# Kernel tuning notes

Hardware: AMD Instinct MI355X
Metric: run time of the kernel (lower is better)

## Reference

```python
import jax, jax.numpy as jnp
import numpy as np
from jax import lax

EPS = 1e-5

def _conv(x, w, pad):
    # x: NCHW, w: OIHW, stride 1
    return lax.conv_general_dilated(x, w, (1, 1), [(pad, pad), (pad, pad)],
                                    dimension_numbers=('NCHW', 'OIHW', 'NCHW'))

def _binconv(x, w):
    # IR-Net/ReActNet HardBinaryConv: sign-binarized weights scaled by per-filter
    # mean |w| (alpha), sign-binarized activations; clip-based STE for backward.
    alpha = jnp.mean(jnp.abs(w), axis=(1, 2, 3), keepdims=True)  # [O,1,1,1]
    wc = jnp.clip(w, -1.0, 1.0)
    bw = lax.stop_gradient(alpha * jnp.sign(w) - wc) + wc
    xc = jnp.clip(x, -1.0, 1.0)
    ba = lax.stop_gradient(jnp.sign(x) - xc) + xc
    return _conv(ba, bw, 1)

def _bn(x, g, b, m, v):
    # inference-mode BatchNorm2d with running stats
    inv = g / jnp.sqrt(v + EPS)
    return x * inv[None, :, None, None] + (b - m * inv)[None, :, None, None]

def _pool(x):
    return lax.reduce_window(x, -jnp.inf, lax.max, (1, 1, 2, 2), (1, 1, 2, 2), 'VALID')

def _htanh(x):
    return jnp.clip(x, -1.0, 1.0)

def setup_inputs() -> dict:
    key = jax.random.key(0)
    ks = jax.random.split(key, 40)
    B = 256
    d = {'x': jax.random.normal(ks[0], (B, 3, 32, 32), jnp.float32)}
    shapes = [(128, 3, 3, 3), (128, 128, 3, 3), (256, 128, 3, 3),
              (256, 256, 3, 3), (512, 256, 3, 3), (512, 512, 3, 3)]
    chans = [128, 128, 256, 256, 512, 512]
    ki = 1
    for i, (ws, c) in enumerate(zip(shapes, chans)):
        fan_in = ws[1] * 9
        d[f'w{i}'] = jax.random.normal(ks[ki], ws, jnp.float32) / np.sqrt(fan_in); ki += 1
        d[f'g{i}'] = jnp.ones((c,), jnp.float32)
        d[f'b{i}'] = jnp.zeros((c,), jnp.float32)
        d[f'm{i}'] = jax.random.normal(ks[ki], (c,), jnp.float32) * 0.1; ki += 1
        d[f'v{i}'] = jax.random.uniform(ks[ki], (c,), jnp.float32, 0.5, 1.5); ki += 1
    d['fcw'] = jax.random.normal(ks[ki], (10, 512 * 4 * 4), jnp.float32) * 0.01
    d['fcb'] = jnp.zeros((10,), jnp.float32)
    return d

def reference(x, w0, g0, b0, m0, v0, w1, g1, b1, m1, v1, w2, g2, b2, m2, v2,
              w3, g3, b3, m3, v3, w4, g4, b4, m4, v4, w5, g5, b5, m5, v5,
              fcw, fcb):
    h = _bn(_conv(x, w0, 1), g0, b0, m0, v0)            # [B,128,32,32]
    h = _htanh(_bn(_pool(_binconv(h, w1)), g1, b1, m1, v1))   # [B,128,16,16]
    h = _htanh(_bn(_binconv(h, w2), g2, b2, m2, v2))          # [B,256,16,16]
    h = _htanh(_bn(_pool(_binconv(h, w3)), g3, b3, m3, v3))   # [B,256,8,8]
    h = _htanh(_bn(_binconv(h, w4), g4, b4, m4, v4))          # [B,512,8,8]
    h = _htanh(_bn(_pool(_binconv(h, w5)), g5, b5, m5, v5))   # [B,512,4,4]
    h = h.reshape(h.shape[0], -1)                             # [B,8192]
    return h @ fcw.T + fcb                                    # [B,10]
```

## Files before the change

kernel.cpp:

```cpp
#include <hip/hip_runtime.h>
#include <cstdint>

#define EPS 1e-5
typedef unsigned long long u64;
typedef unsigned int u32;

struct BnArgs { const float *g[6], *b[6], *m[6], *v[6]; };
struct PackArgs { const float* w[5]; u64* wbt[5]; };

__global__ void bn_prep_all(BnArgs p, double* __restrict__ scale_all,
                            double* __restrict__ shift_all) {
    int i = blockIdx.x * 256 + threadIdx.x;
    if (i >= 1792) return;
    int l, base;
    if (i < 128)       { l = 0; base = 0; }
    else if (i < 256)  { l = 1; base = 128; }
    else if (i < 512)  { l = 2; base = 256; }
    else if (i < 768)  { l = 3; base = 512; }
    else if (i < 1280) { l = 4; base = 768; }
    else               { l = 5; base = 1280; }
    const int c = i - base;
    double inv = (double)p.g[l][c] / sqrt((double)p.v[l][c] + EPS);
    scale_all[i] = inv;
    shift_all[i] = (double)p.b[l][c] - (double)p.m[l][c] * inv;
}

__global__ void zero_out(float* __restrict__ out, int n) {
    int i = blockIdx.x * blockDim.x + threadIdx.x;
    if (i < n) out[i] = 0.f;
}

__global__ void zero_u64(u64* __restrict__ p, size_t n) {
    size_t i = (size_t)blockIdx.x * 256 + threadIdx.x;
    const size_t step = (size_t)gridDim.x * 256;
    for (; i < n; i += step) p[i] = 0ull;
}

__global__ void pack_all(PackArgs pk, const double* __restrict__ scale_all,
                         double* __restrict__ A_all, u32* __restrict__ ct_all) {
    const int ob = blockIdx.x;
    const int t = threadIdx.x;
    int l, base, Cin, bnoff, OTOT, ctoff;
    if (ob < 128)       { l = 0; base = 0;    Cin = 128; bnoff = 128;  OTOT = 128; ctoff = 0; }
    else if (ob < 384)  { l = 1; base = 128;  Cin = 128; bnoff = 256;  OTOT = 256; ctoff = 2048; }
    else if (ob < 640)  { l = 2; base = 384;  Cin = 256; bnoff = 512;  OTOT = 256; ctoff = 6144; }
    else if (ob < 1152) { l = 3; base = 640;  Cin = 256; bnoff = 768;  OTOT = 512; ctoff = 10240; }
    else                { l = 4; base = 1152; Cin = 512; bnoff = 1280; OTOT = 512; ctoff = 18432; }
    const int o = ob - base;
    const float* wo = pk.w[l] + (size_t)o * Cin * 9;

    double s = 0.0;
    for (int k = t; k < Cin * 9; k += 256) s += fabs((double)wo[k]);
    __shared__ double red[256];
    __shared__ u32 stp[9];
    red[t] = s;
    if (t < 9) stp[t] = 0;
    __syncthreads();
    for (int r = 128; r > 0; r >>= 1) {
        if (t < r) red[t] += red[t + r];
        __syncthreads();
    }
    if (t == 0) {
        double alpha = red[0] / (double)(Cin * 9);
        A_all[ob] = alpha * scale_all[bnoff + o];
    }

    const int W64 = Cin / 64;
    u64* wbt = pk.wbt[l];
    for (int e = t; e < 9 * W64; e += 256) {
        int tap = e / W64, word = e % W64;
        u64 bits = 0;
        for (int j = 0; j < 64; ++j) {
            int c = word * 64 + j;
            if (wo[c * 9 + tap] < 0.f) bits |= (1ull << j);
        }
        wbt[((size_t)tap * OTOT + o) * W64 + word] = bits;
        atomicAdd(&stp[tap], (u32)__popcll(bits));
    }
    __syncthreads();

    if (t < 16) {
        const int pat = t;
        int nv = 0;
        u32 cor = 0;
#pragma unroll
        for (int tap = 0; tap < 9; ++tap) {
            const int dy = tap / 3, dx = tap % 3;
            const bool inv = ((pat & 1) && dy == 0) || ((pat & 2) && dy == 2) ||
                             ((pat & 4) && dx == 0) || ((pat & 8) && dx == 2);
            if (inv) cor += stp[tap]; else nv++;
        }
        ct_all[ctoff + pat * OTOT + o] = (u32)(nv * 64 * W64) + 2u * cor;
    }
}

__global__ __launch_bounds__(256) void conv0_pack(
        const float* __restrict__ x, const float* __restrict__ w0,
        const double* __restrict__ scale, const double* __restrict__ shift,
        u64* __restrict__ bits0) {
    __shared__ double wlds[128 * 27];
    __shared__ double sc[128], sh[128];
    const int tid = threadIdx.x;
    for (int e = tid; e < 128 * 27; e += 256) wlds[e] = (double)w0[e];
    for (int e = tid; e < 128; e += 256) { sc[e] = scale[e]; sh[e] = shift[e]; }
    __syncthreads();

    const int n = blockIdx.y;
    const int p = blockIdx.x * 256 + tid;
    const int y = p >> 5, xx = p & 31;
    const float* xn = x + (size_t)n * 3 * 32 * 32;

    double win[27];
#pragma unroll
    for (int c = 0; c < 3; ++c)
#pragma unroll
        for (int dy = 0; dy < 3; ++dy)
#pragma unroll
            for (int dx = 0; dx < 3; ++dx) {
                const int yy = y + dy - 1, xs = xx + dx - 1;
                const bool ok = (yy >= 0 && yy < 32 && xs >= 0 && xs < 32);
                win[(c * 3 + dy) * 3 + dx] = ok ? (double)xn[(c * 32 + yy) * 32 + xs] : 0.0;
            }

    u64* op = bits0 + (((size_t)n * 34 + (y + 1)) * 34 + (xx + 1)) * 2;
#pragma unroll
    for (int og = 0; og < 2; ++og) {
        u64 word = 0;
#pragma unroll 2
        for (int j = 0; j < 64; ++j) {
            const int o = og * 64 + j;
            const double* wo = &wlds[o * 27];
            double acc = 0.0;
#pragma unroll
            for (int k = 0; k < 27; ++k) acc = fma(wo[k], win[k], acc);
            const double val = acc * sc[o] + sh[o];
            word |= (u64)(val < 0.0) << j;
        }
        op[og] = word;
    }
}

template<int H, int W, int W64, int OTOT, bool POOL, bool LAST, int MINW>
__global__ __launch_bounds__(256, MINW) void bconv6(
        const u64* __restrict__ in_bits, const u64* __restrict__ wbt,
        const double* __restrict__ A, const double* __restrict__ B,
        const u32* __restrict__ ct_all, int ctoff,
        u32* __restrict__ out_bits, float* __restrict__ h5) {
    const int tid = threadIdx.x;
    const int wave = tid >> 6, lane = tid & 63;
    constexpr int OPW = 32;
    constexpr int WPI = (H * W) / 64;
    constexpr int IPB = (WPI >= 4) ? 1 : (4 / WPI);
    const int img = (IPB == 1) ? blockIdx.z : blockIdx.z * IPB + wave;
    const int wii = (IPB == 1) ? (blockIdx.y * 4 + wave) : 0;
    const int y = wii * (64 / W) + lane / W;
    const int x = lane % W;
    const int obase = blockIdx.x * OPW;

    __shared__ u64 wl[9 * OPW * W64];
    __shared__ u32 ctl[16 * 33];
    __shared__ double Ald[OPW], Bld[OPW];
    {
        for (int e = tid; e < 9 * OPW * W64; e += 256) {
            const int tap = e / (OPW * W64), r = e % (OPW * W64);
            wl[e] = wbt[((size_t)tap * OTOT + obase) * W64 + r];
        }
        for (int e = tid; e < 16 * OPW; e += 256) {
            const int pat = e >> 5, oc = e & 31;
            ctl[pat * 33 + oc] = ct_all[ctoff + pat * OTOT + obase + oc];
        }
        for (int e = tid; e < OPW; e += 256) {
            Ald[e] = A[obase + e];
            Bld[e] = B[obase + e];
        }
    }
    __syncthreads();

    constexpr int RC = W + 2;
    const u64* ib = in_bits + (size_t)img * (H + 2) * RC * W64;

    int acc[OPW];
#pragma unroll
    for (int i = 0; i < OPW; ++i) acc[i] = 0;

#pragma unroll 1
    for (int dy = 0; dy < 3; ++dy) {
#pragma unroll 1
        for (int dx = 0; dx < 3; ++dx) {
            const u64* q = ib + ((size_t)(y + dy) * RC + (x + dx)) * W64;
            u64 wn[W64];
#pragma unroll
            for (int k = 0; k < W64; ++k) wn[k] = q[k];
            const u64* wt = &wl[(dy * 3 + dx) * OPW * W64];
#pragma unroll
            for (int oc = 0; oc < OPW; ++oc) {
#pragma unroll
                for (int k = 0; k < W64; ++k)
                    acc[oc] += (int)__popcll(wn[k] ^ wt[oc * W64 + k]);
            }
        }
    }

    const int pat = (y == 0 ? 1 : 0) | (y == H - 1 ? 2 : 0) |
                    (x == 0 ? 4 : 0) | (x == W - 1 ? 8 : 0);
    const int ctbase = pat * 33;
    constexpr int Hp = POOL ? H / 2 : H, Wp = POOL ? W / 2 : W;
    const bool writer = (!POOL) || (((lane & 1) == 0) && ((lane & W) == 0));
    const int py = POOL ? (y >> 1) : y, px = POOL ? (x >> 1) : x;

    u32 cur = 0;
#pragma unroll
    for (int oc = 0; oc < OPW; ++oc) {
        int v = (int)ctl[ctbase + oc] - 2 * acc[oc];
        if (POOL) {
            int v2 = max(v, __shfl_xor(v, 1, 64));
            v = max(v2, __shfl_xor(v2, W, 64));
        }
        const double t = fma(Ald[oc], (double)v, Bld[oc]);
        if (LAST) {
            const double hcl = fmin(1.0, fmax(-1.0, t));
            if (writer)
                h5[(((size_t)img * OTOT + obase + oc) * Hp + py) * Wp + px] = (float)hcl;
        } else {
            cur |= (u32)(t < 0.0) << oc;
        }
    }
    if (!LAST && writer) {
        out_bits[(((size_t)img * (Hp + 2) + (py + 1)) * (Wp + 2) + (px + 1)) * (OTOT / 32)
                 + (obase >> 5)] = cur;
    }
}

__global__ void fc_kernel(const float* __restrict__ h, const float* __restrict__ fcw,
                          const float* __restrict__ fcb, float* __restrict__ out) {
    const int n = blockIdx.x, t = threadIdx.x;
    double acc[10];
#pragma unroll
    for (int j = 0; j < 10; ++j) acc[j] = 0.0;
    const float* hn = h + (size_t)n * 8192;
    for (int k = t; k < 8192; k += 256) {
        double xv = (double)hn[k];
#pragma unroll
        for (int j = 0; j < 10; ++j) acc[j] += xv * (double)fcw[j * 8192 + k];
    }
    __shared__ double red[10][256];
#pragma unroll
    for (int j = 0; j < 10; ++j) red[j][t] = acc[j];
    __syncthreads();
    for (int r = 128; r > 0; r >>= 1) {
        if (t < r) {
#pragma unroll
            for (int j = 0; j < 10; ++j) red[j][t] += red[j][t + r];
        }
        __syncthreads();
    }
    if (t < 10) out[n * 10 + t] = (float)(red[t][0] + (double)fcb[t]);
}

extern "C" void kernel_launch(void* const* d_in, const int* in_sizes, int n_in,
                              void* d_out, int out_size, void* d_ws, size_t ws_size,
                              hipStream_t stream) {
    const float* X = (const float*)d_in[0];
    BnArgs bn;
    PackArgs pk;
    const float* Wt0 = (const float*)d_in[1];
    for (int i = 0; i < 6; ++i) {
        bn.g[i] = (const float*)d_in[2 + 5 * i];
        bn.b[i] = (const float*)d_in[3 + 5 * i];
        bn.m[i] = (const float*)d_in[4 + 5 * i];
        bn.v[i] = (const float*)d_in[5 + 5 * i];
    }
    for (int i = 0; i < 5; ++i) pk.w[i] = (const float*)d_in[1 + 5 * (i + 1)];
    const float* fcw = (const float*)d_in[31];
    const float* fcb = (const float*)d_in[32];
    float* out = (float*)d_out;

    char* ws = (char*)d_ws;
    size_t off = 0;
    auto alloc = [&](size_t bytes) -> void* {
        void* p = ws + off;
        off = (off + bytes + 255) & ~(size_t)255;
        return p;
    };

    double* scale_all = (double*)alloc(1792 * sizeof(double));
    double* shift_all = (double*)alloc(1792 * sizeof(double));
    double* A_all     = (double*)alloc(1664 * sizeof(double));
    u32* ct_all       = (u32*)alloc(26624 * sizeof(u32));
    const size_t WBN[5] = {128ull * 9 * 2, 256ull * 9 * 2, 256ull * 9 * 4,
                           512ull * 9 * 4, 512ull * 9 * 8};
    for (int i = 0; i < 5; ++i) pk.wbt[i] = (u64*)alloc(WBN[i] * sizeof(u64));
    u64* bits4 = (u64*)alloc(256ull * 10 * 10 * 8 * sizeof(u64));
    u64* bits0 = (u64*)alloc(256ull * 34 * 34 * 2 * sizeof(u64));
    u64* bits1 = (u64*)alloc(256ull * 18 * 18 * 2 * sizeof(u64));
    u64* bits2 = (u64*)alloc(256ull * 18 * 18 * 4 * sizeof(u64));
    u64* bits3 = (u64*)alloc(256ull * 10 * 10 * 4 * sizeof(u64));
    const size_t bits_u64 =
        256ull * (10 * 10 * 8 + 34 * 34 * 2 + 18 * 18 * 2 + 18 * 18 * 4 + 10 * 10 * 4);
    float* h5 = (float*)bits0;
    {
        const size_t h5_bytes = 256ull * 8192 * sizeof(float);
        const size_t have = (size_t)((char*)(bits3 + 256ull * 10 * 10 * 4) - (char*)bits0);
        if (h5_bytes > have) alloc(h5_bytes - have);
    }

    if (off > ws_size) {
        zero_out<<<dim3((out_size + 255) / 256), dim3(256), 0, stream>>>(out, out_size);
        return;
    }

    const int BOF[6] = {0, 128, 256, 512, 768, 1280};
    const int AOF[5] = {0, 128, 384, 640, 1152};
    const int CTO[5] = {0, 2048, 6144, 10240, 18432};

    bn_prep_all<<<dim3(7), dim3(256), 0, stream>>>(bn, scale_all, shift_all);
    pack_all<<<dim3(1664), dim3(256), 0, stream>>>(pk, scale_all, A_all, ct_all);
    zero_u64<<<dim3(2048), dim3(256), 0, stream>>>(bits4, bits_u64);

    conv0_pack<<<dim3(4, 256), dim3(256), 0, stream>>>(
        X, Wt0, scale_all + BOF[0], shift_all + BOF[0], bits0);

    bconv6<32, 32, 2, 128, true, false, 4><<<dim3(4, 4, 256), dim3(256), 0, stream>>>(
        bits0, pk.wbt[0], A_all + AOF[0], shift_all + BOF[1], ct_all, CTO[0],
        (u32*)bits1, nullptr);
    bconv6<16, 16, 2, 256, false, false, 4><<<dim3(8, 1, 256), dim3(256), 0, stream>>>(
        bits1, pk.wbt[1], A_all + AOF[1], shift_all + BOF[2], ct_all, CTO[1],
        (u32*)bits2, nullptr);
    bconv6<16, 16, 4, 256, true, false, 4><<<dim3(8, 1, 256), dim3(256), 0, stream>>>(
        bits2, pk.wbt[2], A_all + AOF[2], shift_all + BOF[3], ct_all, CTO[2],
        (u32*)bits3, nullptr);
    bconv6<8, 8, 4, 512, false, false, 4><<<dim3(16, 1, 64), dim3(256), 0, stream>>>(
        bits3, pk.wbt[3], A_all + AOF[3], shift_all + BOF[4], ct_all, CTO[3],
        (u32*)bits4, nullptr);
    bconv6<8, 8, 8, 512, true, true, 4><<<dim3(16, 1, 64), dim3(256), 0, stream>>>(
        bits4, pk.wbt[4], A_all + AOF[4], shift_all + BOF[5], ct_all, CTO[4],
        nullptr, h5);

    fc_kernel<<<dim3(256), dim3(256), 0, stream>>>(h5, fcw, fcb, out);
}
```

Measured before the change: 588.2 us.

## Add quad-per-thread pooled last binary conv and narrow layer-4 channel tiles

The last binary conv layer moves to a new kernel in which each thread computes all four pre-pool pixels of one 2x2 window for 4 output channels. This removes the shuffle-based max pooling and the idle non-writer lanes, and gives 2048 blocks instead of 1024. Layer 4 now uses 16 output channels per block with 16-bit packed output stores, which doubles the block count. The cost is more register use (MINW 2) and more redundant loads of input windows.

After: 609.9 us. 1.04x slower.

```diff
diff --git a/kernel.cpp b/kernel.cpp
--- a/kernel.cpp
+++ b/kernel.cpp
@@ -4,6 +4,7 @@
 #define EPS 1e-5
 typedef unsigned long long u64;
 typedef unsigned int u32;
+typedef unsigned short u16;
 
 struct BnArgs { const float *g[6], *b[6], *m[6], *v[6]; };
 struct PackArgs { const float* w[5]; u64* wbt[5]; };
@@ -140,15 +141,14 @@
     }
 }
 
-template<int H, int W, int W64, int OTOT, bool POOL, bool LAST, int MINW>
+template<int H, int W, int W64, int OTOT, int OPW, bool POOL, int MINW>
 __global__ __launch_bounds__(256, MINW) void bconv6(
         const u64* __restrict__ in_bits, const u64* __restrict__ wbt,
         const double* __restrict__ A, const double* __restrict__ B,
         const u32* __restrict__ ct_all, int ctoff,
-        u32* __restrict__ out_bits, float* __restrict__ h5) {
+        u32* __restrict__ out_bits) {
     const int tid = threadIdx.x;
     const int wave = tid >> 6, lane = tid & 63;
-    constexpr int OPW = 32;
     constexpr int WPI = (H * W) / 64;
     constexpr int IPB = (WPI >= 4) ? 1 : (4 / WPI);
     const int img = (IPB == 1) ? blockIdx.z : blockIdx.z * IPB + wave;
@@ -158,7 +158,7 @@
     const int obase = blockIdx.x * OPW;
 
     __shared__ u64 wl[9 * OPW * W64];
-    __shared__ u32 ctl[16 * 33];
+    __shared__ u32 ctl[16 * (OPW + 1)];
     __shared__ double Ald[OPW], Bld[OPW];
     {
         for (int e = tid; e < 9 * OPW * W64; e += 256) {
@@ -166,8 +166,8 @@
             wl[e] = wbt[((size_t)tap * OTOT + obase) * W64 + r];
         }
         for (int e = tid; e < 16 * OPW; e += 256) {
-            const int pat = e >> 5, oc = e & 31;
-            ctl[pat * 33 + oc] = ct_all[ctoff + pat * OTOT + obase + oc];
+            const int pat = e / OPW, oc = e % OPW;
+            ctl[pat * (OPW + 1) + oc] = ct_all[ctoff + pat * OTOT + obase + oc];
         }
         for (int e = tid; e < OPW; e += 256) {
             Ald[e] = A[obase + e];
@@ -203,7 +203,7 @@
 
     const int pat = (y == 0 ? 1 : 0) | (y == H - 1 ? 2 : 0) |
                     (x == 0 ? 4 : 0) | (x == W - 1 ? 8 : 0);
-    const int ctbase = pat * 33;
+    const int ctbase = pat * (OPW + 1);
     constexpr int Hp = POOL ? H / 2 : H, Wp = POOL ? W / 2 : W;
     const bool writer = (!POOL) || (((lane & 1) == 0) && ((lane & W) == 0));
     const int py = POOL ? (y >> 1) : y, px = POOL ? (x >> 1) : x;
@@ -217,17 +217,106 @@
             v = max(v2, __shfl_xor(v2, W, 64));
         }
         const double t = fma(Ald[oc], (double)v, Bld[oc]);
-        if (LAST) {
-            const double hcl = fmin(1.0, fmax(-1.0, t));
-            if (writer)
-                h5[(((size_t)img * OTOT + obase + oc) * Hp + py) * Wp + px] = (float)hcl;
-        } else {
-            cur |= (u32)(t < 0.0) << oc;
-        }
-    }
-    if (!LAST && writer) {
-        out_bits[(((size_t)img * (Hp + 2) + (py + 1)) * (Wp + 2) + (px + 1)) * (OTOT / 32)
-                 + (obase >> 5)] = cur;
+        cur |= (u32)(t < 0.0) << oc;
+    }
+    if (writer) {
+        const size_t pixbase = ((size_t)img * (Hp + 2) + (py + 1)) * (Wp + 2) + (px + 1);
+        if (OPW == 32)
+            out_bits[pixbase * (OTOT / 32) + (obase >> 5)] = cur;
+        else
+            ((u16*)out_bits)[pixbase * (OTOT / 16) + (obase >> 4)] = (u16)cur;
+    }
+}
+
+template<int MINW>
+__global__ __launch_bounds__(256, MINW) void bconv_quad(
+        const u64* __restrict__ in_bits, const u64* __restrict__ wbt,
+        const double* __restrict__ A, const double* __restrict__ B,
+        const u32* __restrict__ ct_all, int ctoff,
+        float* __restrict__ h5) {
+    constexpr int W64 = 8, OTOT = 512, OPW = 4;
+    const int tid = threadIdx.x;
+    const int wave = tid >> 6, lane = tid & 63;
+    const int img = blockIdx.y * 16 + wave * 4 + (lane >> 4);
+    const int quad = lane & 15;
+    const int py = quad >> 2, px = quad & 3;
+    const int obase = blockIdx.x * OPW;
+
+    __shared__ u64 wl[9 * OPW * W64];
+    __shared__ u32 ctl[16 * (OPW + 1)];
+    __shared__ double Ald[OPW], Bld[OPW];
+    for (int e = tid; e < 9 * OPW * W64; e += 256) {
+        const int tap = e / (OPW * W64), r = e % (OPW * W64);
+        wl[e] = wbt[((size_t)tap * OTOT + obase) * W64 + r];
+    }
+    if (tid < 16 * OPW) {
+        const int pat = tid / OPW, oc = tid % OPW;
+        ctl[pat * (OPW + 1) + oc] = ct_all[ctoff + pat * OTOT + obase + oc];
+    }
+    if (tid < OPW) { Ald[tid] = A[obase + tid]; Bld[tid] = B[obase + tid]; }
+    __syncthreads();
+
+    const u64* ib = in_bits + (size_t)img * 10 * 10 * W64;
+
+    int acc[4][OPW];
+#pragma unroll
+    for (int p = 0; p < 4; ++p)
+#pragma unroll
+        for (int oc = 0; oc < OPW; ++oc) acc[p][oc] = 0;
+
+#pragma unroll 1
+    for (int dy = 0; dy < 3; ++dy) {
+#pragma unroll 1
+        for (int dx = 0; dx < 3; ++dx) {
+            u64 win[2][2][W64];
+#pragma unroll
+            for (int p = 0; p < 2; ++p)
+#pragma unroll
+                for (int q = 0; q < 2; ++q) {
+                    const u64* src = ib + ((size_t)(2 * py + p + dy) * 10 +
+                                           (2 * px + q + dx)) * W64;
+#pragma unroll
+                    for (int k = 0; k < W64; ++k) win[p][q][k] = src[k];
+                }
+            const u64* wt = &wl[(dy * 3 + dx) * OPW * W64];
+#pragma unroll
+            for (int oc = 0; oc < OPW; ++oc) {
+                u64 w[W64];
+#pragma unroll
+                for (int k = 0; k < W64; ++k) w[k] = wt[oc * W64 + k];
+#pragma unroll
+                for (int p = 0; p < 2; ++p)
+#pragma unroll
+                    for (int q = 0; q < 2; ++q) {
+                        int tp = 0;
+#pragma unroll
+                        for (int k = 0; k < W64; ++k)
+                            tp += (int)__popcll(win[p][q][k] ^ w[k]);
+                        acc[p * 2 + q][oc] += tp;
+                    }
+            }
+        }
+    }
+
+    int patp[4];
+#pragma unroll
+    for (int p = 0; p < 2; ++p)
+#pragma unroll
+        for (int q = 0; q < 2; ++q) {
+            const int cy = 2 * py + p, cx = 2 * px + q;
+            patp[p * 2 + q] = (cy == 0 ? 1 : 0) | (cy == 7 ? 2 : 0) |
+                              (cx == 0 ? 4 : 0) | (cx == 7 ? 8 : 0);
+        }
+
+#pragma unroll
+    for (int oc = 0; oc < OPW; ++oc) {
+        int v = (int)ctl[patp[0] * (OPW + 1) + oc] - 2 * acc[0][oc];
+        v = max(v, (int)ctl[patp[1] * (OPW + 1) + oc] - 2 * acc[1][oc]);
+        v = max(v, (int)ctl[patp[2] * (OPW + 1) + oc] - 2 * acc[2][oc]);
+        v = max(v, (int)ctl[patp[3] * (OPW + 1) + oc] - 2 * acc[3][oc]);
+        const double t = fma(Ald[oc], (double)v, Bld[oc]);
+        const double hcl = fmin(1.0, fmax(-1.0, t));
+        h5[(((size_t)img * OTOT + obase + oc) * 4 + py) * 4 + px] = (float)hcl;
     }
 }
 
@@ -320,21 +409,16 @@
     conv0_pack<<<dim3(4, 256), dim3(256), 0, stream>>>(
         X, Wt0, scale_all + BOF[0], shift_all + BOF[0], bits0);
 
-    bconv6<32, 32, 2, 128, true, false, 4><<<dim3(4, 4, 256), dim3(256), 0, stream>>>(
-        bits0, pk.wbt[0], A_all + AOF[0], shift_all + BOF[1], ct_all, CTO[0],
-        (u32*)bits1, nullptr);
-    bconv6<16, 16, 2, 256, false, false, 4><<<dim3(8, 1, 256), dim3(256), 0, stream>>>(
-        bits1, pk.wbt[1], A_all + AOF[1], shift_all + BOF[2], ct_all, CTO[1],
-        (u32*)bits2, nullptr);
-    bconv6<16, 16, 4, 256, true, false, 4><<<dim3(8, 1, 256), dim3(256), 0, stream>>>(
-        bits2, pk.wbt[2], A_all + AOF[2], shift_all + BOF[3], ct_all, CTO[2],
-        (u32*)bits3, nullptr);
-    bconv6<8, 8, 4, 512, false, false, 4><<<dim3(16, 1, 64), dim3(256), 0, stream>>>(
-        bits3, pk.wbt[3], A_all + AOF[3], shift_all + BOF[4], ct_all, CTO[3],
-        (u32*)bits4, nullptr);
-    bconv6<8, 8, 8, 512, true, true, 4><<<dim3(16, 1, 64), dim3(256), 0, stream>>>(
-        bits4, pk.wbt[4], A_all + AOF[4], shift_all + BOF[5], ct_all, CTO[4],
-        nullptr, h5);
+    bconv6<32, 32, 2, 128, 32, true, 4><<<dim3(4, 4, 256), dim3(256), 0, stream>>>(
+        bits0, pk.wbt[0], A_all + AOF[0], shift_all + BOF[1], ct_all, CTO[0], (u32*)bits1);
+    bconv6<16, 16, 2, 256, 32, false, 4><<<dim3(8, 1, 256), dim3(256), 0, stream>>>(
+        bits1, pk.wbt[1], A_all + AOF[1], shift_all + BOF[2], ct_all, CTO[1], (u32*)bits2);
+    bconv6<16, 16, 4, 256, 32, true, 4><<<dim3(8, 1, 256), dim3(256), 0, stream>>>(
+        bits2, pk.wbt[2], A_all + AOF[2], shift_all + BOF[3], ct_all, CTO[2], (u32*)bits3);
+    bconv6<8, 8, 4, 512, 16, false, 4><<<dim3(32, 1, 64), dim3(256), 0, stream>>>(
+        bits3, pk.wbt[3], A_all + AOF[3], shift_all + BOF[4], ct_all, CTO[3], (u32*)bits4);
+    bconv_quad<2><<<dim3(128, 16), dim3(256), 0, stream>>>(
+        bits4, pk.wbt[4], A_all + AOF[4], shift_all + BOF[5], ct_all, CTO[4], h5);
 
     fc_kernel<<<dim3(256), dim3(256), 0, stream>>>(h5, fcw, fcb, out);
 }
```
